# Kernel optimization log

Hardware: AMD Instinct MI355X
Metric: run time of the kernel (lower is better)

Reference implementation:

```python
import jax, jax.numpy as jnp
import numpy as np

V, D, T_BLK, H, HS = 50257, 512, 2048, 8, 64
B, T = 2, 2048


def setup_inputs() -> dict:
    key = jax.random.key(0)
    ks = jax.random.split(key, 12)
    s = 0.02
    return {
        "idx": jax.random.randint(ks[0], (B, T), 0, V),
        "targets": jax.random.randint(ks[1], (B, T), 0, V),
        "tok_emb": jax.random.normal(ks[2], (V, D), jnp.float32) * s,
        "pos_emb": jax.random.normal(ks[3], (T_BLK, D), jnp.float32) * s,
        "wq": jax.random.normal(ks[4], (H, D, HS), jnp.float32) * s,
        "wk": jax.random.normal(ks[5], (H, D, HS), jnp.float32) * s,
        "wv": jax.random.normal(ks[6], (H, D, HS), jnp.float32) * s,
        "w1": jax.random.normal(ks[7], (D, D), jnp.float32) * s,
        "b1": jnp.zeros((D,), jnp.float32),
        "w_head": jax.random.normal(ks[8], (D, V), jnp.float32) * s,
        "b_head": jnp.zeros((V,), jnp.float32),
    }


def _forward(idx, targets, tok_emb, pos_emb, wq, wk, wv, w1, b1, w_head, b_head):
    b, t = idx.shape
    x = tok_emb[idx] + pos_emb[:t]                        # [B,T,D]
    # batched per-head QKV (equivalent to the per-head Linear loop)
    q = jnp.einsum("btd,hde->bhte", x, wq)                # [B,H,T,hs]
    k = jnp.einsum("btd,hde->bhte", x, wk)
    v = jnp.einsum("btd,hde->bhte", x, wv)
    scores = jnp.einsum("bhte,bhse->bhts", q, k) / jnp.sqrt(jnp.float32(HS))
    causal = jnp.tril(jnp.ones((t, t), bool))
    scores = jnp.where(causal, scores, -jnp.inf)
    weights = jax.nn.softmax(scores, axis=-1)
    att = jnp.einsum("bhts,bhse->bhte", weights, v)       # [B,H,T,hs]
    att = att.transpose(0, 2, 1, 3).reshape(b, t, H * HS)  # head-concat order
    x_ff = jax.nn.relu(att @ w1 + b1)                      # [B,T,D]
    logits = x_ff @ w_head + b_head                        # [B,T,V]
    logp = jax.nn.log_softmax(logits, axis=-1)
    loss = -jnp.mean(jnp.take_along_axis(logp, targets[..., None], axis=-1))
    return logits, loss


def reference(idx, targets, tok_emb, pos_emb, wq, wk, wv, w1, b1, w_head, b_head):
    return _forward(idx, targets, tok_emb, pos_emb, wq, wk, wv, w1, b1, w_head, b_head)
```

## Files before the change

### kernel.cpp

```cpp
#include <hip/hip_runtime.h>
#include <hip/hip_bf16.h>
#include <hip/hip_fp8.h>
#include <stdint.h>

#define V_SZ   50257
#define NPAD   50432
#define NT_HEAD 197
#define D_SZ   512
#define HS_SZ  64
#define H_N    8
#define T_SZ   2048
#define ROWS   4096

typedef __bf16 bf16x8 __attribute__((ext_vector_type(8)));
typedef __bf16 bf16x4 __attribute__((ext_vector_type(4)));
typedef float  f32x4  __attribute__((ext_vector_type(4)));
typedef long   l64x2  __attribute__((ext_vector_type(2)));

__device__ __forceinline__ unsigned char to_fp8(float x) {
  __hip_fp8_e4m3 t(x);
  return t.__x;
}

__device__ __forceinline__ void gload_lds16(const void* g, void* l) {
  auto gp = (const __attribute__((address_space(1))) uint32_t*)(uintptr_t)g;
  auto lp = (__attribute__((address_space(3))) uint32_t*)(uintptr_t)l;
  __builtin_amdgcn_global_load_lds(gp, lp, 16, 0, 0);
}

__global__ __launch_bounds__(256) void k_embed(const int* __restrict__ idx,
    const float* __restrict__ tok, const float* __restrict__ pos,
    __bf16* __restrict__ xb) {
  const int row = blockIdx.x;
  const int tpos = row & (T_SZ - 1);
  const int tokid = idx[row];
  const int d = threadIdx.x * 2;
  float2 tv = *(const float2*)(tok + (size_t)tokid * D_SZ + d);
  float2 pv = *(const float2*)(pos + (size_t)tpos * D_SZ + d);
  __bf16* o = xb + (size_t)row * D_SZ + d;
  o[0] = (__bf16)(tv.x + pv.x);
  o[1] = (__bf16)(tv.y + pv.y);
}

__global__ __launch_bounds__(256) void k_prep_wqkv(const float* __restrict__ wq,
    const float* __restrict__ wk, const float* __restrict__ wv, __bf16* __restrict__ dst) {
  const int id = blockIdx.x * 256 + threadIdx.x;
  const int n = id >> 9, dd = id & 511;
  const int mi = n >> 9, rem = n & 511, h = rem >> 6, e = rem & 63;
  const float* src = (mi == 0) ? wq : ((mi == 1) ? wk : wv);
  dst[id] = (__bf16)src[((size_t)h * D_SZ + dd) * HS_SZ + e];
}

__global__ __launch_bounds__(256) void k_prep_w1(const float* __restrict__ w1,
                                                 __bf16* __restrict__ dst) {
  const int id = blockIdx.x * 256 + threadIdx.x;
  const int n = id >> 9, kk = id & 511;
  dst[id] = (__bf16)w1[(size_t)kk * D_SZ + n];
}

__global__ void k_prep_wh(const float* __restrict__ wh, unsigned char* __restrict__ dst) {
  __shared__ float tile[32][33];
  const int n0 = blockIdx.x * 32, d0 = blockIdx.y * 32;
  const int tx = threadIdx.x, ty = threadIdx.y;
  #pragma unroll
  for (int i = 0; i < 4; ++i) {
    int dd = d0 + ty + i * 8, n = n0 + tx;
    tile[ty + i * 8][tx] = (n < V_SZ) ? wh[(size_t)dd * V_SZ + n] : 0.f;
  }
  __syncthreads();
  #pragma unroll
  for (int i = 0; i < 4; ++i) {
    int n = n0 + ty + i * 8, dd = d0 + tx;
    dst[(size_t)n * D_SZ + dd] = to_fp8(tile[tx][ty + i * 8] * 256.f);
  }
}

template <int EPI>
__global__ __launch_bounds__(256) void k_gemm(const __bf16* __restrict__ A,
    const __bf16* __restrict__ Bt, const float* __restrict__ bias,
    unsigned char* __restrict__ outA8, __bf16* __restrict__ outK, __bf16* __restrict__ outV) {
  __shared__ __bf16 As[128 * 32];
  __shared__ __bf16 Bs[128 * 32];
  const int t = threadIdx.x, lane = t & 63, w = t >> 6;
  const int wr = w >> 1, wc = w & 1;
  const int m0 = blockIdx.x * 128, n0 = blockIdx.y * 128;
  const int srow = lane >> 2, k8 = (lane & 3) * 8;

  f32x4 zero = {0.f, 0.f, 0.f, 0.f};
  f32x4 acc[4][4];
  #pragma unroll
  for (int mm = 0; mm < 4; ++mm)
    #pragma unroll
    for (int nn = 0; nn < 4; ++nn) acc[mm][nn] = zero;

  const __bf16* Ag = A  + (size_t)(m0 + w * 16 + srow) * D_SZ + k8;
  const __bf16* Bg = Bt + (size_t)(n0 + w * 16 + srow) * D_SZ + k8;
  char* AsB = (char*)As + w * 1024;
  char* BsB = (char*)Bs + w * 1024;
  const int kslot = (lane >> 4) * 8;
  const int arow = wr * 64 + (lane & 15);
  const int brow = wc * 64 + (lane & 15);

  for (int kt = 0; kt < 16; ++kt) {
    const int k0 = kt * 32;
    gload_lds16(Ag + k0,             AsB);
    gload_lds16(Ag + 64 * D_SZ + k0, AsB + 4096);
    gload_lds16(Bg + k0,             BsB);
    gload_lds16(Bg + 64 * D_SZ + k0, BsB + 4096);
    __syncthreads();

    bf16x8 af[4], bfr[4];
    #pragma unroll
    for (int mm = 0; mm < 4; ++mm)
      af[mm] = *(const bf16x8*)(As + (arow + mm * 16) * 32 + kslot);
    #pragma unroll
    for (int nn = 0; nn < 4; ++nn)
      bfr[nn] = *(const bf16x8*)(Bs + (brow + nn * 16) * 32 + kslot);
    #pragma unroll
    for (int mm = 0; mm < 4; ++mm)
      #pragma unroll
      for (int nn = 0; nn < 4; ++nn)
        acc[mm][nn] = __builtin_amdgcn_mfma_f32_16x16x32_bf16(af[mm], bfr[nn], acc[mm][nn], 0, 0, 0);
    __syncthreads();
  }

  const int lrow = (lane >> 4) * 4, lcol = lane & 15;
  #pragma unroll
  for (int mm = 0; mm < 4; ++mm) {
    #pragma unroll
    for (int nn = 0; nn < 4; ++nn) {
      const int grow0 = m0 + wr * 64 + mm * 16 + lrow;
      const int gcol  = n0 + wc * 64 + nn * 16 + lcol;
      if (EPI == 0) {
        const int mi = gcol >> 9, rem = gcol & 511, hh = rem >> 6, e = rem & 63;
        const int bb = grow0 >> 11, tt0 = grow0 & 2047;
        const int bhh = bb * H_N + hh;
        if (mi == 2) {
          bf16x4 pk = { (__bf16)acc[mm][nn][0], (__bf16)acc[mm][nn][1],
                        (__bf16)acc[mm][nn][2], (__bf16)acc[mm][nn][3] };
          *(bf16x4*)(outV + ((size_t)bhh * HS_SZ + e) * T_SZ + tt0) = pk;
        } else {
          __bf16* dq = (mi == 0 ? (__bf16*)outA8 : outK) + ((size_t)bhh * T_SZ + tt0) * HS_SZ + e;
          const float sc = (mi == 0) ? 0.125f : 1.f;
          #pragma unroll
          for (int j = 0; j < 4; ++j) dq[(size_t)j * HS_SZ] = (__bf16)(acc[mm][nn][j] * sc);
        }
      } else {
        #pragma unroll
        for (int j = 0; j < 4; ++j) {
          float xv = acc[mm][nn][j] + bias[gcol];
          xv = (xv > 0.f ? xv : 0.f) * 256.f;
          outA8[(size_t)(grow0 + j) * D_SZ + gcol] = to_fp8(xv);
        }
      }
    }
  }
}

__global__ __launch_bounds__(512, 4) void k_ghead(const unsigned char* __restrict__ A,
    const unsigned char* __restrict__ Bt, const float* __restrict__ bias,
    float* __restrict__ logits, float2* __restrict__ part) {
  __shared__ char lds[49152];
  const int t = threadIdx.x, lane = t & 63, w = t >> 6;
  const int wr = w >> 2, wc = w & 3;
  const int m0 = blockIdx.x * 128, n0 = blockIdx.y * 256;
  const int lm = lane & 15, g = lane >> 4;
  const int r2 = lane >> 2, c2 = lane & 3;
  const int csw2 = (c2 ^ ((r2 >> 1) & 3)) << 4;

  f32x4 acc[4][4];
  #pragma unroll
  for (int mm = 0; mm < 4; ++mm)
    #pragma unroll
    for (int nn = 0; nn < 4; ++nn) acc[mm][nn] = f32x4{0.f, 0.f, 0.f, 0.f};

  const unsigned char* Ab = A  + (size_t)m0 * D_SZ;
  const unsigned char* Bb = Bt + (size_t)n0 * D_SZ;

  auto STAGE = [&](int buf, int kt) {
    char* Al = lds + buf * 24576;
    char* Bl = Al + 8192;
    gload_lds16(Ab + (size_t)(w * 16 + r2) * D_SZ + kt * 64 + csw2,        Al + w * 1024);
    gload_lds16(Bb + (size_t)(w * 16 + r2) * D_SZ + kt * 64 + csw2,        Bl + w * 1024);
    gload_lds16(Bb + (size_t)(128 + w * 16 + r2) * D_SZ + kt * 64 + csw2,  Bl + 8192 + w * 1024);
  };

  STAGE(0, 0);
  STAGE(1, 1);
  asm volatile("s_waitcnt vmcnt(3)" ::: "memory");
  __builtin_amdgcn_s_barrier();
  asm volatile("" ::: "memory");

  for (int kt = 0; kt < 8; ++kt) {
    const char* Al = lds + (kt & 1) * 24576;
    const char* Bl = Al + 8192;
    l64x2 b2[4];
    #pragma unroll
    for (int nn = 0; nn < 4; ++nn) {
      const int row = wc * 64 + nn * 16 + lm;
      b2[nn] = *(const l64x2*)(Bl + row * 64 + ((g ^ ((row >> 1) & 3)) << 4));
    }
    #pragma unroll
    for (int mm = 0; mm < 4; ++mm) {
      const int row = wr * 64 + mm * 16 + lm;
      l64x2 a2 = *(const l64x2*)(Al + row * 64 + ((g ^ ((row >> 1) & 3)) << 4));
      #pragma unroll
      for (int nn = 0; nn < 4; ++nn)
        acc[mm][nn] = __builtin_amdgcn_mfma_f32_16x16x32_fp8_fp8(a2.x, b2[nn].x, acc[mm][nn], 0, 0, 0);
      #pragma unroll
      for (int nn = 0; nn < 4; ++nn)
        acc[mm][nn] = __builtin_amdgcn_mfma_f32_16x16x32_fp8_fp8(a2.y, b2[nn].y, acc[mm][nn], 0, 0, 0);
    }
    if (kt == 7) break;
    __builtin_amdgcn_s_barrier();
    asm volatile("" ::: "memory");
    if (kt < 6) {
      STAGE(kt & 1, kt + 2);
      asm volatile("s_waitcnt vmcnt(3)" ::: "memory");
    } else {
      asm volatile("s_waitcnt vmcnt(0)" ::: "memory");
    }
    __builtin_amdgcn_s_barrier();
    asm volatile("" ::: "memory");
  }
  __syncthreads();

  const float SC = 1.f / 65536.f;
  float* tr   = (float*)lds;
  float* redS = tr + 32 * 260;
  const int colL = wc * 64 + lm;
  float bj[4]; int vok[4];
  #pragma unroll
  for (int nn = 0; nn < 4; ++nn) {
    const int gc = n0 + colL + nn * 16;
    vok[nn] = (gc < V_SZ);
    bj[nn] = vok[nn] ? bias[gc] : 0.f;
  }
  const int r32s = t >> 4, c16 = t & 15;
  #pragma unroll
  for (int mm = 0; mm < 4; ++mm) {
    if (mm) __syncthreads();
    float sj[4];
    #pragma unroll
    for (int j = 0; j < 4; ++j) {
      const int r32 = wr * 16 + g * 4 + j;
      float s = 0.f;
      #pragma unroll
      for (int nn = 0; nn < 4; ++nn) {
        const float v = acc[mm][nn][j] * SC + bj[nn];
        tr[r32 * 260 + colL + nn * 16] = v;
        if (vok[nn]) s += __expf(v);
      }
      sj[j] = s;
    }
    #pragma unroll
    for (int j = 0; j < 4; ++j) {
      float s = sj[j];
      s += __shfl_xor(s, 1); s += __shfl_xor(s, 2);
      s += __shfl_xor(s, 4); s += __shfl_xor(s, 8);
      if (lm == 0) redS[(wr * 64 + mm * 16 + g * 4 + j) * 4 + wc] = s;
    }
    __syncthreads();
    const int grow = m0 + (r32s >> 4) * 64 + mm * 16 + (r32s & 15);
    float* gp = logits + (size_t)grow * V_SZ;
    #pragma unroll
    for (int i = 0; i < 4; ++i) {
      const int c4 = c16 + 16 * i;
      const int gc0 = n0 + c4 * 4;
      f32x4 vv = *(const f32x4*)(tr + r32s * 260 + c4 * 4);
      if (gc0 + 3 < V_SZ) {
        *(f32x4*)(gp + gc0) = vv;
      } else {
        if (gc0     < V_SZ) gp[gc0]     = vv.x;
        if (gc0 + 1 < V_SZ) gp[gc0 + 1] = vv.y;
        if (gc0 + 2 < V_SZ) gp[gc0 + 2] = vv.z;
        if (gc0 + 3 < V_SZ) gp[gc0 + 3] = vv.w;
      }
    }
  }
  __syncthreads();
  if (t < 128) {
    const float S = redS[t * 4] + redS[t * 4 + 1] + redS[t * 4 + 2] + redS[t * 4 + 3];
    part[(size_t)(m0 + t) * NT_HEAD + blockIdx.y] = float2{0.f, S};
  }
}

__global__ __launch_bounds__(256) void k_attn(const __bf16* __restrict__ qbf,
    const __bf16* __restrict__ kbf, const __bf16* __restrict__ vbf,
    __bf16* __restrict__ xatt) {
  const int qt = 31 - blockIdx.x;
  const int bh = blockIdx.y;
  const int b = bh >> 3, h = bh & 7;
  const int t = threadIdx.x, lane = t & 63, w = t >> 6;
  const int qr = lane & 15, g = lane >> 4, r7 = qr & 7;
  __shared__ __bf16 Klds[2][64 * 64];
  __shared__ __bf16 Vt[2][64 * 64];
  __shared__ __bf16 Plds[4][16 * 72];

  const int qglob = qt * 64 + w * 16 + qr;
  const __bf16* qrow_g = qbf + ((size_t)bh * T_SZ + qglob) * HS_SZ + g * 8;
  const bf16x8 qf0 = *(const bf16x8*)(qrow_g);
  const bf16x8 qf1 = *(const bf16x8*)(qrow_g + 32);
  asm volatile("s_waitcnt vmcnt(0)" ::: "memory");

  f32x4 att[4];
  #pragma unroll
  for (int n = 0; n < 4; ++n) att[n] = f32x4{0.f, 0.f, 0.f, 0.f};
  float m = -3.0e38f, l = 0.f;

  const char* Kg = (const char*)(kbf + (size_t)bh * T_SZ * HS_SZ);
  const char* Vg = (const char*)(vbf + (size_t)bh * HS_SZ * T_SZ);
  const int r8 = lane >> 3, cc = lane & 7;
  const int csw = ((cc ^ r8) << 4);

  auto STAGE = [&](int bsel, int kt2) {
    char* Kb = (char*)&Klds[bsel][0] + w * 2048;
    char* Vb = (char*)&Vt[bsel][0] + w * 2048;
    const char* ks = Kg + (size_t)(kt2 * 64 + w * 16) * 128;
    gload_lds16(ks + r8 * 128 + csw,        Kb);
    gload_lds16(ks + 1024 + r8 * 128 + csw, Kb + 1024);
    const char* vs = Vg + (size_t)(w * 16) * (T_SZ * 2) + kt2 * 128;
    gload_lds16(vs + r8 * (T_SZ * 2) + csw,       Vb);
    gload_lds16(vs + (8 + r8) * (T_SZ * 2) + csw, Vb + 1024);
  };

  STAGE(0, 0);
  if (qt >= 1) {
    STAGE(1, 1);
    asm volatile("s_waitcnt vmcnt(4)" ::: "memory");
  } else {
    asm volatile("s_waitcnt vmcnt(0)" ::: "memory");
  }
  __builtin_amdgcn_s_barrier();
  asm volatile("" ::: "memory");

  for (int kt = 0; kt <= qt; ++kt) {
    const int bs = kt & 1;
    const __bf16* Kl = &Klds[bs][0];
    const __bf16* Vl = &Vt[bs][0];
    const bool diag = (kt == qt);
    f32x4 acc[4];
    #pragma unroll
    for (int a = 0; a < 4; ++a) {
      if (diag && a > w) {
        acc[a] = f32x4{-3.0e38f, -3.0e38f, -3.0e38f, -3.0e38f};
      } else {
        const char* kb = (const char*)Kl + (a * 16 + qr) * 128;
        bf16x8 ka0 = *(const bf16x8*)(kb + ((g ^ r7) << 4));
        bf16x8 ka1 = *(const bf16x8*)(kb + (((g + 4) ^ r7) << 4));
        f32x4 z = {0.f, 0.f, 0.f, 0.f};
        __builtin_amdgcn_s_setprio(1);
        z = __builtin_amdgcn_mfma_f32_16x16x32_bf16(ka0, qf0, z, 0, 0, 0);
        z = __builtin_amdgcn_mfma_f32_16x16x32_bf16(ka1, qf1, z, 0, 0, 0);
        __builtin_amdgcn_s_setprio(0);
        acc[a] = z;
      }
    }
    if (diag) {
      #pragma unroll
      for (int a = 0; a < 4; ++a)
        #pragma unroll
        for (int j = 0; j < 4; ++j)
          if (a * 16 + g * 4 + j > w * 16 + qr) acc[a][j] = -3.0e38f;
    }

    float mloc = -3.0e38f;
    #pragma unroll
    for (int a = 0; a < 4; ++a)
      #pragma unroll
      for (int j = 0; j < 4; ++j) mloc = fmaxf(mloc, acc[a][j]);
    mloc = fmaxf(mloc, __shfl_xor(mloc, 16));
    mloc = fmaxf(mloc, __shfl_xor(mloc, 32));
    const float newm = fmaxf(m, mloc);
    const float alpha = __expf(m - newm);
    float lloc = 0.f;
    #pragma unroll
    for (int a = 0; a < 4; ++a) {
      float p0 = __expf(acc[a][0] - newm);
      float p1 = __expf(acc[a][1] - newm);
      float p2 = __expf(acc[a][2] - newm);
      float p3 = __expf(acc[a][3] - newm);
      lloc += (p0 + p1) + (p2 + p3);
      bf16x4 pw = { (__bf16)p0, (__bf16)p1, (__bf16)p2, (__bf16)p3 };
      *(bf16x4*)((char*)&Plds[w][0] + qr * 144 + (a * 16 + g * 4) * 2) = pw;
    }
    lloc += __shfl_xor(lloc, 16);
    lloc += __shfl_xor(lloc, 32);
    l = l * alpha + lloc;
    m = newm;

    #pragma unroll
    for (int j = 0; j < 4; ++j) {
      const float aj = __shfl(alpha, g * 4 + j);
      #pragma unroll
      for (int n = 0; n < 4; ++n) att[n][j] *= aj;
    }

    #pragma unroll
    for (int c = 0; c < 2; ++c) {
      bf16x8 pa = *(const bf16x8*)((const char*)&Plds[w][0] + qr * 144 + c * 64 + g * 16);
      __builtin_amdgcn_s_setprio(1);
      #pragma unroll
      for (int n = 0; n < 4; ++n) {
        const int vrow = n * 16 + qr;
        bf16x8 vb = *(const bf16x8*)((const char*)Vl + vrow * 128 + (((c * 4 + g) ^ r7) << 4));
        att[n] = __builtin_amdgcn_mfma_f32_16x16x32_bf16(pa, vb, att[n], 0, 0, 0);
      }
      __builtin_amdgcn_s_setprio(0);
    }

    if (kt == qt) break;
    __builtin_amdgcn_s_barrier();
    asm volatile("" ::: "memory");
    if (kt + 2 <= qt) {
      STAGE(bs, kt + 2);
      asm volatile("s_waitcnt vmcnt(4)" ::: "memory");
    } else {
      asm volatile("s_waitcnt vmcnt(0)" ::: "memory");
    }
    __builtin_amdgcn_s_barrier();
    asm volatile("" ::: "memory");
  }

  #pragma unroll
  for (int j = 0; j < 4; ++j) {
    const float lj = __shfl(l, g * 4 + j);
    const float inv = 1.f / lj;
    const int row = qt * 64 + w * 16 + g * 4 + j;
    __bf16* orow = xatt + ((size_t)(b * T_SZ + row)) * D_SZ + h * HS_SZ + qr;
    #pragma unroll
    for (int n = 0; n < 4; ++n) orow[n * 16] = (__bf16)(att[n][j] * inv);
  }
}

__global__ __launch_bounds__(256) void k_lsemerge(const float2* __restrict__ part,
                                                  float* __restrict__ lse) {
  const int row = blockIdx.x * 4 + (threadIdx.x >> 6);
  const int lane = threadIdx.x & 63;
  const float2* pr = part + (size_t)row * NT_HEAD;
  float M = -3.0e38f, S = 0.f;
  for (int i = lane; i < NT_HEAD; i += 64) {
    float2 p = pr[i];
    float nm = fmaxf(M, p.x);
    S = S * __expf(M - nm) + p.y * __expf(p.x - nm);
    M = nm;
  }
  #pragma unroll
  for (int off = 1; off < 64; off <<= 1) {
    float Mo = __shfl_xor(M, off), So = __shfl_xor(S, off);
    float nm = fmaxf(M, Mo);
    S = S * __expf(M - nm) + So * __expf(Mo - nm);
    M = nm;
  }
  if (lane == 0) lse[row] = M + __logf(S);
}

__global__ __launch_bounds__(256) void k_loss(const float* __restrict__ logits,
    const float* __restrict__ lse, const int* __restrict__ tgt,
    float* __restrict__ outloss) {
  float acc = 0.f;
  for (int r = threadIdx.x; r < ROWS; r += 256)
    acc += lse[r] - logits[(size_t)r * V_SZ + tgt[r]];
  #pragma unroll
  for (int off = 32; off > 0; off >>= 1) acc += __shfl_down(acc, off);
  __shared__ float pw[4];
  if ((threadIdx.x & 63) == 0) pw[threadIdx.x >> 6] = acc;
  __syncthreads();
  if (threadIdx.x == 0) outloss[0] = (pw[0] + pw[1] + pw[2] + pw[3]) * (1.f / ROWS);
}

extern "C" void kernel_launch(void* const* d_in, const int* in_sizes, int n_in,
                              void* d_out, int out_size, void* d_ws, size_t ws_size,
                              hipStream_t stream) {
  const int*   idx = (const int*)d_in[0];
  const int*   tgt = (const int*)d_in[1];
  const float* tok = (const float*)d_in[2];
  const float* pos = (const float*)d_in[3];
  const float* wq  = (const float*)d_in[4];
  const float* wk  = (const float*)d_in[5];
  const float* wv  = (const float*)d_in[6];
  const float* w1  = (const float*)d_in[7];
  const float* b1  = (const float*)d_in[8];
  const float* wh  = (const float*)d_in[9];
  const float* bh  = (const float*)d_in[10];

  float* logits = (float*)d_out;
  float* lossp  = logits + (size_t)ROWS * V_SZ;

  char* ws = (char*)d_ws;
  __bf16* xb   = (__bf16*)(ws + 0);
  __bf16* Bqkv = (__bf16*)(ws + (4u  << 20));
  __bf16* B1t  = (__bf16*)(ws + (11u << 19));
  __bf16* qbf  = (__bf16*)(ws + (6u  << 20));
  __bf16* kbf  = (__bf16*)(ws + (10u << 20));
  __bf16* vbf  = (__bf16*)(ws + (14u << 20));
  float2* part = (float2*)(ws + 0);
  float*  lse  = (float*) (ws + (20u << 20));
  __bf16* xatt = (__bf16*)(ws + (30u << 20));
  unsigned char* Aff8 = (unsigned char*)(ws + (34u << 20));
  unsigned char* Wht8 = (unsigned char*)(ws + (38u << 20));

  k_embed    <<<ROWS, 256, 0, stream>>>(idx, tok, pos, xb);
  k_prep_wqkv<<<3072, 256, 0, stream>>>(wq, wk, wv, Bqkv);
  k_prep_w1  <<<1024, 256, 0, stream>>>(w1, B1t);
  k_prep_wh  <<<dim3(NPAD / 32, 16), dim3(32, 8), 0, stream>>>(wh, Wht8);

  k_gemm<0><<<dim3(32, 12),  256, 0, stream>>>(xb,   Bqkv, nullptr, (unsigned char*)qbf, kbf, vbf);
  k_attn   <<<dim3(32, 16),  256, 0, stream>>>(qbf, kbf, vbf, xatt);
  k_gemm<1><<<dim3(32, 4),   256, 0, stream>>>(xatt, B1t,  b1,  Aff8, nullptr, nullptr);
  k_ghead  <<<dim3(32, NT_HEAD), 512, 0, stream>>>(Aff8, Wht8, bh, logits, part);

  k_lsemerge<<<ROWS / 4, 256, 0, stream>>>(part, lse);
  k_loss    <<<1,        256, 0, stream>>>(logits, lse, tgt, lossp);
}
```

Baseline: 488.3 us.

## Double-buffer bf16 GEMM with swizzled LDS and triple-buffer fp8 head GEMM

Rewrites the bf16 QKV/FFN GEMM mainloop to stage 64-wide K tiles into a double-buffered, XOR-swizzled 64KB LDS region with async global-to-LDS loads and vmcnt-based waits, instead of single-buffered 32-wide tiles with full syncthreads. The head GEMM moves from double to triple buffering so loads run further ahead of the MFMA work. The aim is to hide global-load latency and reduce bank conflicts and barriers. The cost is more LDS per block (64KB and 72KB), which may lower occupancy, especially for the head kernel declared with 4 blocks per CU.

```diff
diff --git a/kernel.cpp b/kernel.cpp
--- a/kernel.cpp
+++ b/kernel.cpp
@@ -79,49 +79,71 @@
 __global__ __launch_bounds__(256) void k_gemm(const __bf16* __restrict__ A,
     const __bf16* __restrict__ Bt, const float* __restrict__ bias,
     unsigned char* __restrict__ outA8, __bf16* __restrict__ outK, __bf16* __restrict__ outV) {
-  __shared__ __bf16 As[128 * 32];
-  __shared__ __bf16 Bs[128 * 32];
+  __shared__ char lds[65536];
   const int t = threadIdx.x, lane = t & 63, w = t >> 6;
   const int wr = w >> 1, wc = w & 1;
   const int m0 = blockIdx.x * 128, n0 = blockIdx.y * 128;
-  const int srow = lane >> 2, k8 = (lane & 3) * 8;
-
-  f32x4 zero = {0.f, 0.f, 0.f, 0.f};
+  const int r8 = lane >> 3, cc = lane & 7;
+  const int lm = lane & 15, g = lane >> 4, l7 = lane & 7;
+  const int csw = (cc ^ r8) << 4;
+  const int srow8 = w * 8 + r8;
+
   f32x4 acc[4][4];
   #pragma unroll
   for (int mm = 0; mm < 4; ++mm)
     #pragma unroll
-    for (int nn = 0; nn < 4; ++nn) acc[mm][nn] = zero;
-
-  const __bf16* Ag = A  + (size_t)(m0 + w * 16 + srow) * D_SZ + k8;
-  const __bf16* Bg = Bt + (size_t)(n0 + w * 16 + srow) * D_SZ + k8;
-  char* AsB = (char*)As + w * 1024;
-  char* BsB = (char*)Bs + w * 1024;
-  const int kslot = (lane >> 4) * 8;
-  const int arow = wr * 64 + (lane & 15);
-  const int brow = wc * 64 + (lane & 15);
-
-  for (int kt = 0; kt < 16; ++kt) {
-    const int k0 = kt * 32;
-    gload_lds16(Ag + k0,             AsB);
-    gload_lds16(Ag + 64 * D_SZ + k0, AsB + 4096);
-    gload_lds16(Bg + k0,             BsB);
-    gload_lds16(Bg + 64 * D_SZ + k0, BsB + 4096);
-    __syncthreads();
-
-    bf16x8 af[4], bfr[4];
-    #pragma unroll
-    for (int mm = 0; mm < 4; ++mm)
-      af[mm] = *(const bf16x8*)(As + (arow + mm * 16) * 32 + kslot);
-    #pragma unroll
-    for (int nn = 0; nn < 4; ++nn)
-      bfr[nn] = *(const bf16x8*)(Bs + (brow + nn * 16) * 32 + kslot);
-    #pragma unroll
-    for (int mm = 0; mm < 4; ++mm)
+    for (int nn = 0; nn < 4; ++nn) acc[mm][nn] = f32x4{0.f, 0.f, 0.f, 0.f};
+
+  const char* Ab = (const char*)A  + (size_t)m0 * (D_SZ * 2);
+  const char* Bb = (const char*)Bt + (size_t)n0 * (D_SZ * 2);
+
+  auto STAGE = [&](int buf, int kt) {
+    char* Al = lds + buf * 32768;
+    const char* Asrc = Ab + kt * 128;
+    const char* Bsrc = Bb + kt * 128;
+    #pragma unroll
+    for (int i = 0; i < 4; ++i) {
+      gload_lds16(Asrc + (size_t)(i * 32 + srow8) * 1024 + csw, Al + (i * 32 + w * 8) * 128);
+      gload_lds16(Bsrc + (size_t)(i * 32 + srow8) * 1024 + csw, Al + 16384 + (i * 32 + w * 8) * 128);
+    }
+  };
+
+  STAGE(0, 0);
+  STAGE(1, 1);
+  asm volatile("s_waitcnt vmcnt(8)" ::: "memory");
+  __builtin_amdgcn_s_barrier();
+  asm volatile("" ::: "memory");
+
+  for (int kt = 0; kt < 8; ++kt) {
+    const char* Al = lds + (kt & 1) * 32768;
+    const char* Bl = Al + 16384;
+    #pragma unroll
+    for (int kh = 0; kh < 2; ++kh) {
+      const int ch = ((kh * 4 + g) ^ l7) << 4;
+      bf16x8 a[4], b[4];
+      #pragma unroll
+      for (int mm = 0; mm < 4; ++mm)
+        a[mm] = *(const bf16x8*)(Al + (wr * 64 + mm * 16 + lm) * 128 + ch);
       #pragma unroll
       for (int nn = 0; nn < 4; ++nn)
-        acc[mm][nn] = __builtin_amdgcn_mfma_f32_16x16x32_bf16(af[mm], bfr[nn], acc[mm][nn], 0, 0, 0);
-    __syncthreads();
+        b[nn] = *(const bf16x8*)(Bl + (wc * 64 + nn * 16 + lm) * 128 + ch);
+      #pragma unroll
+      for (int mm = 0; mm < 4; ++mm)
+        #pragma unroll
+        for (int nn = 0; nn < 4; ++nn)
+          acc[mm][nn] = __builtin_amdgcn_mfma_f32_16x16x32_bf16(a[mm], b[nn], acc[mm][nn], 0, 0, 0);
+    }
+    if (kt == 7) break;
+    __builtin_amdgcn_s_barrier();
+    asm volatile("" ::: "memory");
+    if (kt < 6) {
+      STAGE(kt & 1, kt + 2);
+      asm volatile("s_waitcnt vmcnt(8)" ::: "memory");
+    } else {
+      asm volatile("s_waitcnt vmcnt(0)" ::: "memory");
+    }
+    __builtin_amdgcn_s_barrier();
+    asm volatile("" ::: "memory");
   }
 
   const int lrow = (lane >> 4) * 4, lcol = lane & 15;
@@ -160,7 +182,7 @@
 __global__ __launch_bounds__(512, 4) void k_ghead(const unsigned char* __restrict__ A,
     const unsigned char* __restrict__ Bt, const float* __restrict__ bias,
     float* __restrict__ logits, float2* __restrict__ part) {
-  __shared__ char lds[49152];
+  __shared__ char lds[73728];
   const int t = threadIdx.x, lane = t & 63, w = t >> 6;
   const int wr = w >> 2, wc = w & 3;
   const int m0 = blockIdx.x * 128, n0 = blockIdx.y * 256;
@@ -187,12 +209,14 @@
 
   STAGE(0, 0);
   STAGE(1, 1);
-  asm volatile("s_waitcnt vmcnt(3)" ::: "memory");
+  STAGE(2, 2);
+  asm volatile("s_waitcnt vmcnt(6)" ::: "memory");
   __builtin_amdgcn_s_barrier();
   asm volatile("" ::: "memory");
 
   for (int kt = 0; kt < 8; ++kt) {
-    const char* Al = lds + (kt & 1) * 24576;
+    const int bi = kt % 3;
+    const char* Al = lds + bi * 24576;
     const char* Bl = Al + 8192;
     l64x2 b2[4];
     #pragma unroll
@@ -214,8 +238,10 @@
     if (kt == 7) break;
     __builtin_amdgcn_s_barrier();
     asm volatile("" ::: "memory");
-    if (kt < 6) {
-      STAGE(kt & 1, kt + 2);
+    if (kt + 3 < 8) {
+      STAGE(bi, kt + 3);
+      asm volatile("s_waitcnt vmcnt(6)" ::: "memory");
+    } else if (kt + 2 < 8) {
       asm volatile("s_waitcnt vmcnt(3)" ::: "memory");
     } else {
       asm volatile("s_waitcnt vmcnt(0)" ::: "memory");
```

After: 474.6 us (median of 2 runs). -2.8%, faster.
